# Kernel tuning notes

Measured on AMD Instinct MI355X. Metric: run time of the kernel, lower is better.

Reference implementation:

```python
import jax, jax.numpy as jnp
import numpy as np

SR = 44100
SEQ_DUR = 6.0
FBINS = 113
FMIN = 91.6
NSGT_SCALE = 100.0
MIN_WIN = 4


def _mel_frequencies(fmin, fmax, bnds):
    # MelScale from the nsgt package
    hz2mel = lambda f: 1127.01048 * np.log(f / 700.0 + 1.0)
    mel2hz = lambda m: (np.exp(m / 1127.01048) - 1.0) * 700.0
    mmin, mmax = hz2mel(fmin), hz2mel(fmax)
    mbnd = (mmax - mmin) / (bnds - 1)
    return mel2hz(np.arange(bnds) * mbnd + mmin)


def _hannwin(l):
    # fft-centered hann window (peak at index 0), as in nsgt.util.hannwin
    r = np.arange(l, dtype=np.float64) * (2.0 * np.pi / l)
    return 0.5 * (np.cos(r) + 1.0)


def _build_nsgt_params(Ls):
    """Replicates nsgfwin(sliced=False) + calcwinrange + matrixform nsgtf layout.
    Returns G[n_bins, maxLg] (window values, zero where padded) and
    idx[n_bins, maxLg] (gather indices into the length-Ls spectrum)."""
    f = _mel_frequencies(FMIN, SR / 2.0, FBINS)
    nf = SR / 2.0
    lim = int(np.argmax(f > 0))
    if lim != 0:
        f = f[lim:]
    lim = int(np.argmax(f >= nf))
    if lim != 0:
        f = f[:lim]
    lbas = len(f)
    frqs = np.concatenate(((0.0,), f, (nf,)))
    fbas = np.concatenate((frqs, SR - frqs[-2:0:-1]))
    fbas *= float(Ls) / SR
    # bandwidths M[k] (samples)
    M = np.zeros(fbas.shape, dtype=np.int64)
    M[0] = np.round(2 * fbas[1])
    for k in range(1, 2 * lbas + 1):
        M[k] = np.round(fbas[k + 1] - fbas[k - 1])
    M[-1] = np.round(Ls - fbas[-2])
    M = np.clip(M, MIN_WIN, None)
    g = [_hannwin(m) for m in M]
    fbas[lbas] = (fbas[lbas - 1] + fbas[lbas + 1]) / 2
    fbas[lbas + 2] = Ls - fbas[lbas]
    rfbas = np.round(fbas).astype(np.int64)  # window center positions (= timepos)
    # real=True, reducedform=0 -> keep bins 0 .. len(g)//2 (DC..Nyquist)
    n_bins = len(g) // 2 + 1
    maxLg = int(M.max())  # matrixform: every bin padded (in the middle) to max bandwidth
    idx = np.zeros((n_bins, maxLg), dtype=np.int32)
    G = np.zeros((n_bins, maxLg), dtype=np.float32)
    for j in range(n_bins):
        gj = g[j]
        Lg = len(gj)
        tp = int(rfbas[j])
        h = (Lg + 1) // 2  # positive-frequency half
        nh = Lg // 2       # negative-frequency half
        idx[j, :h] = (tp + np.arange(h)) % Ls
        G[j, :h] = gj[:h]
        if nh > 0:
            idx[j, maxLg - nh:] = (tp - nh + np.arange(nh)) % Ls
            G[j, maxLg - nh:] = gj[h:]
    return G, idx


def setup_inputs() -> dict:
    key = jax.random.key(0)
    S, C = 16, 2
    Ls = int(SEQ_DUR * SR)
    x = jax.random.normal(key, (S, C, Ls), dtype=jnp.float32)
    G, idx = _build_nsgt_params(Ls)
    return {"x": x, "G": jnp.asarray(G), "idx": jnp.asarray(idx)}


def reference(x, G, idx):
    # x: (S, C, Ls); G, idx: (n_bins, maxLg)
    S, C, T = x.shape
    ft = jnp.fft.fft(x.reshape(S * C, T))      # (N, Ls) complex64
    c = ft[:, idx] * G                         # (N, n_bins, maxLg): windowed spectrum slices
    coefs = jnp.fft.ifft(c, axis=-1)           # per-bin time frames (matrixform NSGT coeffs)
    coefs = coefs.reshape(S, C, c.shape[1], c.shape[2])
    # torch.view_as_real + * NSGT_SCALE
    return jnp.stack([coefs.real, coefs.imag], axis=-1) * NSGT_SCALE
```

## Files before the change

### kernel.cpp

```cpp
#include <hip/hip_runtime.h>

#define TPB 256
#define TPF 1024
constexpr int LS = 264600;
constexpr int N1 = 525;
constexpr int N2 = 504;
constexpr int ROWS = 32;
constexpr int M_FFT = 16384;
constexpr float TWO_PI_F = 6.28318530717958647692f;
constexpr float PI_F     = 3.14159265358979323846f;

__device__ __forceinline__ int rev7(int x) { return (int)(__brev((unsigned)x) >> 25); }
__device__ __forceinline__ float2 cmul(float2 a, float2 b) {
    return make_float2(a.x * b.x - a.y * b.y, a.x * b.y + a.y * b.x);
}
__device__ __forceinline__ int sidx(int hi, int lo) {
    return (hi << 7) + (lo ^ (hi & 15));
}

__global__ void k0_scan(const float* __restrict__ G, int NL, int* __restrict__ hnh) {
    const int j = blockIdx.x;
    __shared__ int s_first, s_last;
    if (threadIdx.x == 0) { s_first = NL; s_last = -1; }
    __syncthreads();
    const float* Gj = G + (size_t)j * NL;
    for (int m = threadIdx.x; m < NL; m += blockDim.x) {
        if (Gj[m] == 0.0f) {
            atomicMin(&s_first, m);
            atomicMax(&s_last, m);
        }
    }
    __syncthreads();
    if (threadIdx.x == 0) {
        int h  = s_first;
        int nh = (s_last >= 0) ? (NL - 1 - s_last) : 0;
        hnh[2 * j]     = h;
        hnh[2 * j + 1] = nh;
    }
}

__global__ __launch_bounds__(TPB) void k1_dft525(const float* __restrict__ x,
                                                 float2* __restrict__ A) {
    const int n2 = blockIdx.x;
    const int r  = blockIdx.y;
    __shared__ float  xs[N1];
    __shared__ float2 ys[N1];
    __shared__ float2 w25[25];
    __shared__ float2 w21[21];
    const float* xr = x + (size_t)r * LS + n2;
    for (int t = threadIdx.x; t < N1; t += TPB) {
        xs[t] = xr[(size_t)t * N2];
    }
    if (threadIdx.x < 25) {
        float a = -TWO_PI_F * (float)threadIdx.x / 25.0f;
        float s, c; sincosf(a, &s, &c);
        w25[threadIdx.x] = make_float2(c, s);
    } else if (threadIdx.x >= 32 && threadIdx.x < 53) {
        int k = threadIdx.x - 32;
        float a = -TWO_PI_F * (float)k / 21.0f;
        float s, c; sincosf(a, &s, &c);
        w21[k] = make_float2(c, s);
    }
    __syncthreads();
    for (int i = threadIdx.x; i < N1; i += TPB) {
        int alpha = i % 25, b = i / 25;
        float re = 0.f, im = 0.f;
        int iw = 0, it = b;
        #pragma unroll
        for (int a = 0; a < 25; ++a) {
            float  v = xs[it];
            float2 w = w25[iw];
            re = fmaf(v, w.x, re);
            im = fmaf(v, w.y, im);
            it += 21;
            iw += alpha; if (iw >= 25) iw -= 25;
        }
        float ang = -TWO_PI_F * (float)(b * alpha) / (float)N1;
        float s, c; sincosf(ang, &s, &c);
        ys[i] = make_float2(re * c - im * s, re * s + im * c);
    }
    __syncthreads();
    for (int k = threadIdx.x; k < N1; k += TPB) {
        int alpha = k % 25, beta = k / 25;
        float re = 0.f, im = 0.f;
        int iw = 0, iy = alpha;
        #pragma unroll
        for (int b = 0; b < 21; ++b) {
            float2 v = ys[iy];
            float2 w = w21[iw];
            re = fmaf(v.x, w.x, re); re = fmaf(-v.y, w.y, re);
            im = fmaf(v.x, w.y, im); im = fmaf( v.y, w.x, im);
            iy += 25;
            iw += beta; if (iw >= 21) iw -= 21;
        }
        float ang = -TWO_PI_F * (float)(k * n2) / (float)LS;
        float s, c; sincosf(ang, &s, &c);
        A[((size_t)r * N1 + k) * N2 + n2] = make_float2(re * c - im * s, re * s + im * c);
    }
}

__global__ __launch_bounds__(TPB) void k2_dft504(float2* __restrict__ A) {
    const int k1 = blockIdx.x;
    const int r  = blockIdx.y;
    __shared__ float2 as[N2];
    __shared__ float2 ys[N2];
    __shared__ float2 w21[21];
    __shared__ float2 w24[24];
    float2* row = A + ((size_t)r * N1 + k1) * N2;
    for (int t = threadIdx.x; t < N2; t += TPB) as[t] = row[t];
    if (threadIdx.x < 21) {
        float a = -TWO_PI_F * (float)threadIdx.x / 21.0f;
        float s, c; sincosf(a, &s, &c);
        w21[threadIdx.x] = make_float2(c, s);
    } else if (threadIdx.x >= 32 && threadIdx.x < 56) {
        int k = threadIdx.x - 32;
        float a = -TWO_PI_F * (float)k / 24.0f;
        float s, c; sincosf(a, &s, &c);
        w24[k] = make_float2(c, s);
    }
    __syncthreads();
    for (int i = threadIdx.x; i < N2; i += TPB) {
        int alpha = i % 21, b = i / 21;
        float re = 0.f, im = 0.f;
        int iw = 0, it = b;
        #pragma unroll
        for (int a = 0; a < 21; ++a) {
            float2 v = as[it];
            float2 w = w21[iw];
            re = fmaf(v.x, w.x, re); re = fmaf(-v.y, w.y, re);
            im = fmaf(v.x, w.y, im); im = fmaf( v.y, w.x, im);
            it += 24;
            iw += alpha; if (iw >= 21) iw -= 21;
        }
        float ang = -TWO_PI_F * (float)(b * alpha) / (float)N2;
        float s, c; sincosf(ang, &s, &c);
        ys[i] = make_float2(re * c - im * s, re * s + im * c);
    }
    __syncthreads();
    for (int k = threadIdx.x; k < N2; k += TPB) {
        int alpha = k % 21, beta = k / 21;
        float re = 0.f, im = 0.f;
        int iw = 0, iy = alpha;
        #pragma unroll
        for (int b = 0; b < 24; ++b) {
            float2 v = ys[iy];
            float2 w = w24[iw];
            re = fmaf(v.x, w.x, re); re = fmaf(-v.y, w.y, re);
            im = fmaf(v.x, w.y, im); im = fmaf( v.y, w.x, im);
            iy += 21;
            iw += beta; if (iw >= 24) iw -= 24;
        }
        row[k] = make_float2(re, im);
    }
}

__global__ void k_setup(float2* __restrict__ kc, float2* __restrict__ bchirp,
                        float2* __restrict__ twg, int NL) {
    int t = blockIdx.x * blockDim.x + threadIdx.x;
    long long twoNL = 2LL * NL;
    if (t < M_FFT) {
        long long d = 0; bool act = false;
        if (t < NL)              { d = t;        act = true; }
        else if (t > M_FFT - NL) { d = t - M_FFT; act = true; }
        float2 v = make_float2(0.f, 0.f);
        if (act) {
            long long ph = (d * d) % twoNL;
            float th = -PI_F * (float)ph / (float)NL;
            float s, c; sincosf(th, &s, &c);
            v = make_float2(c, s);
        }
        kc[t] = v;
    } else {
        int n = t - M_FFT;
        if (n < NL) {
            long long ph = ((long long)n * n) % twoNL;
            float th = PI_F * (float)ph / (float)NL;
            float s, c; sincosf(th, &s, &c);
            bchirp[n] = make_float2(c, s);
        } else if (n < NL + 64) {
            int q = n - NL;
            float th = -TWO_PI_F * (float)q / 128.0f;
            float s, c; sincosf(th, &s, &c);
            twg[q] = make_float2(c, s);
        }
    }
}

__device__ void fft128_dif(float2 (*ld)[129], const float2* tw, int f, int q) {
    for (int ls = 6; ls >= 0; --ls) {
        int span = 1 << ls;
        for (int b = q; b < 64; b += 16) {
            int j = b & (span - 1);
            int g = b >> ls;
            int u = (g << (ls + 1)) + j;
            int v = u + span;
            float2 A = ld[f][u], B = ld[f][v];
            float2 s = make_float2(A.x + B.x, A.y + B.y);
            float2 d = make_float2(A.x - B.x, A.y - B.y);
            ld[f][u] = s;
            ld[f][v] = cmul(d, tw[j << (6 - ls)]);
        }
        __syncthreads();
    }
}

#define FFT_PROLOG                                                        \
    __shared__ float2 ld[16][129];                                        \
    __shared__ float2 tw[64];                                             \
    if (threadIdx.x < 64) {                                               \
        float th = -TWO_PI_F * (float)threadIdx.x / 128.0f;               \
        float s, c; sincosf(th, &s, &c);                                  \
        tw[threadIdx.x] = make_float2(c, s);                              \
    }

__global__ __launch_bounds__(TPB) void kfft_cols_fwd(float2* __restrict__ P) {
    const int cg = blockIdx.x;
    const size_t vb = (size_t)blockIdx.y * M_FFT;
    FFT_PROLOG
    const int c0 = cg * 16;
    for (int i = threadIdx.x; i < 2048; i += TPB) {
        int cl = i & 15, r = i >> 4;
        ld[cl][r] = P[vb + (c0 + cl) + 128 * r];
    }
    __syncthreads();
    fft128_dif(ld, tw, threadIdx.x >> 4, threadIdx.x & 15);
    for (int i = threadIdx.x; i < 2048; i += TPB) {
        int cl = i & 15, pos = i >> 4;
        int c = c0 + cl;
        int k1 = rev7(pos);
        float th = -TWO_PI_F * (float)(c * k1) / (float)M_FFT;
        float s, co; sincosf(th, &s, &co);
        P[vb + c + 128 * pos] = cmul(ld[cl][pos], make_float2(co, s));
    }
}

__global__ __launch_bounds__(TPB) void kfft_rows_fwd(float2* __restrict__ P) {
    const int rg = blockIdx.x;
    const size_t vb = (size_t)blockIdx.y * M_FFT;
    FFT_PROLOG
    const int R0 = rg * 16;
    for (int i = threadIdx.x; i < 2048; i += TPB) {
        int fl = i >> 7, c = i & 127;
        ld[fl][c] = P[vb + (size_t)(R0 + fl) * 128 + c];
    }
    __syncthreads();
    fft128_dif(ld, tw, threadIdx.x >> 4, threadIdx.x & 15);
    for (int i = threadIdx.x; i < 2048; i += TPB) {
        int fl = i >> 7, pos = i & 127;
        P[vb + (size_t)(R0 + fl) * 128 + pos] = ld[fl][pos];
    }
}

__global__ __launch_bounds__(TPF) void k_fused(const float* __restrict__ Gm,
        const int* __restrict__ idxp, const float2* __restrict__ A,
        const int* __restrict__ hnh, const float2* __restrict__ bchirp,
        const float2* __restrict__ KF, const float2* __restrict__ twg,
        float2* __restrict__ out, int NB, int NL) {
    extern __shared__ float2 mp[];
    const int tid = threadIdx.x;
    const int vg = blockIdx.x;
    const int r = vg / NB, j = vg % NB;
    const int h = hnh[2 * j], nh = hnh[2 * j + 1];
    const int tail0 = NL - nh;
    const float* Gj = Gm + (size_t)j * NL;
    const int*   ij = idxp + (size_t)j * NL;
    const float2* Ar = A + (size_t)r * LS;

    for (int i = tid; i < M_FFT; i += TPF) {
        float2 val = make_float2(0.f, 0.f);
        if (i < h || (i >= tail0 && i < NL)) {
            int k = ij[i];
            float2 f = Ar[(size_t)(k % N1) * N2 + (k / N1)];
            float  g = Gj[i];
            val = cmul(make_float2(f.x * g, f.y * g), bchirp[i]);
        }
        mp[sidx(i >> 7, i & 127)] = val;
    }
    __syncthreads();

    for (int ls = 6; ls >= 0; --ls) {
        const int span = 1 << ls;
        for (int w = tid; w < 8192; w += TPF) {
            const int lo = w & 127, b = w >> 7;
            const int jj = b & (span - 1), g = b >> ls;
            const int u = (g << (ls + 1)) + jj, v = u + span;
            float2 Aa = mp[sidx(u, lo)], Bb = mp[sidx(v, lo)];
            float2 s = make_float2(Aa.x + Bb.x, Aa.y + Bb.y);
            float2 d = make_float2(Aa.x - Bb.x, Aa.y - Bb.y);
            mp[sidx(u, lo)] = s;
            mp[sidx(v, lo)] = cmul(d, twg[jj << (6 - ls)]);
        }
        __syncthreads();
    }
    for (int i = tid; i < M_FFT; i += TPF) {
        const int c = i & 127, pos = i >> 7;
        const int k1 = rev7(pos);
        float th = -TWO_PI_F * (float)(c * k1) / (float)M_FFT;
        float s, co; sincosf(th, &s, &co);
        const int p = sidx(pos, c);
        mp[p] = cmul(mp[p], make_float2(co, s));
    }
    __syncthreads();
    for (int ls = 6; ls >= 0; --ls) {
        const int span = 1 << ls;
        for (int w = tid; w < 8192; w += TPF) {
            const int hi = w & 127, b = w >> 7;
            const int jj = b & (span - 1), g = b >> ls;
            const int u = (g << (ls + 1)) + jj, v = u + span;
            float2 Aa = mp[sidx(hi, u)], Bb = mp[sidx(hi, v)];
            float2 s = make_float2(Aa.x + Bb.x, Aa.y + Bb.y);
            float2 d = make_float2(Aa.x - Bb.x, Aa.y - Bb.y);
            mp[sidx(hi, u)] = s;
            mp[sidx(hi, v)] = cmul(d, twg[jj << (6 - ls)]);
        }
        __syncthreads();
    }
    for (int i = tid; i < M_FFT; i += TPF) {
        const int p = sidx(i >> 7, i & 127);
        mp[p] = cmul(mp[p], KF[i]);
    }
    __syncthreads();
    for (int ls = 0; ls <= 6; ++ls) {
        const int span = 1 << ls;
        for (int w = tid; w < 8192; w += TPF) {
            const int hi = w & 127, b = w >> 7;
            const int jj = b & (span - 1), g = b >> ls;
            const int u = (g << (ls + 1)) + jj, v = u + span;
            float2 wv = twg[jj << (6 - ls)]; wv.y = -wv.y;
            float2 Aa = mp[sidx(hi, u)];
            float2 t  = cmul(mp[sidx(hi, v)], wv);
            mp[sidx(hi, u)] = make_float2(Aa.x + t.x, Aa.y + t.y);
            mp[sidx(hi, v)] = make_float2(Aa.x - t.x, Aa.y - t.y);
        }
        __syncthreads();
    }
    for (int i = tid; i < M_FFT; i += TPF) {
        const int pos = i & 127, R = i >> 7;
        const int k1 = rev7(R);
        float th = TWO_PI_F * (float)(k1 * pos) / (float)M_FFT;
        float s, co; sincosf(th, &s, &co);
        const int p = sidx(R, pos);
        mp[p] = cmul(mp[p], make_float2(co, s));
    }
    __syncthreads();
    for (int ls = 0; ls <= 6; ++ls) {
        const int span = 1 << ls;
        for (int w = tid; w < 8192; w += TPF) {
            const int lo = w & 127, b = w >> 7;
            const int jj = b & (span - 1), g = b >> ls;
            const int u = (g << (ls + 1)) + jj, v = u + span;
            float2 wv = twg[jj << (6 - ls)]; wv.y = -wv.y;
            float2 Aa = mp[sidx(u, lo)];
            float2 t  = cmul(mp[sidx(v, lo)], wv);
            mp[sidx(u, lo)] = make_float2(Aa.x + t.x, Aa.y + t.y);
            mp[sidx(v, lo)] = make_float2(Aa.x - t.x, Aa.y - t.y);
        }
        __syncthreads();
    }
    const float sc = 100.0f / ((float)NL * (float)M_FFT);
    float2* outv = out + (size_t)vg * NL;
    for (int n = tid; n < NL; n += TPF) {
        float2 y = cmul(mp[sidx(n >> 7, n & 127)], bchirp[n]);
        outv[n] = make_float2(y.x * sc, y.y * sc);
    }
}

__global__ __launch_bounds__(TPB) void k3_idft(const float* __restrict__ G,
                                               const int*  __restrict__ idxp,
                                               const float2* __restrict__ FT,
                                               const int*  __restrict__ hnh,
                                               float2* __restrict__ out,
                                               int NB, int NL) {
    extern __shared__ float2 cls[];
    const int j = blockIdx.x;
    const int r = blockIdx.y;
    const int h  = hnh[2 * j];
    const int nh = hnh[2 * j + 1];
    const int Lg = h + nh;
    const float* Gj = G    + (size_t)j * NL;
    const int*   ij = idxp + (size_t)j * NL;

    for (int t = threadIdx.x; t < Lg; t += TPB) {
        int m = (t < h) ? t : (NL - nh + (t - h));
        int k = ij[m];
        float2 f = FT[((size_t)r * N1 + (k % N1)) * N2 + (k / N1)];
        float  g = Gj[m];
        cls[t] = make_float2(f.x * g, f.y * g);
    }
    __syncthreads();

    const float scale = 100.0f / (float)NL;
    const float w0 = TWO_PI_F / (float)NL;
    float2* outr = out + ((size_t)r * NB + j) * NL;

    for (int n_base = 0; n_base < NL; n_base += 4 * TPB) {
        int   n[4];
        float are[4], aim[4], twr[4], twi[4], str[4], sti[4];
        #pragma unroll
        for (int u = 0; u < 4; ++u) {
            n[u] = n_base + u * TPB + (int)threadIdx.x;
            are[u] = 0.f; aim[u] = 0.f;
            float s, c; sincosf(w0 * (float)(n[u] % NL), &s, &c);
            str[u] = c; sti[u] = s;
            twr[u] = 1.f; twi[u] = 0.f;
        }
        for (int t = 0; t < h; ++t) {
            if ((t & 255) == 0) {
                #pragma unroll
                for (int u = 0; u < 4; ++u) {
                    int mm = (int)(((long long)t * (long long)n[u]) % NL);
                    float s, c; sincosf(w0 * (float)mm, &s, &c);
                    twr[u] = c; twi[u] = s;
                }
            }
            float2 cv = cls[t];
            #pragma unroll
            for (int u = 0; u < 4; ++u) {
                are[u] = fmaf(cv.x, twr[u], are[u]);
                are[u] = fmaf(-cv.y, twi[u], are[u]);
                aim[u] = fmaf(cv.x, twi[u], aim[u]);
                aim[u] = fmaf(cv.y, twr[u], aim[u]);
                float nr = twr[u] * str[u] - twi[u] * sti[u];
                float ni = twr[u] * sti[u] + twi[u] * str[u];
                twr[u] = nr; twi[u] = ni;
            }
        }
        const int m0 = NL - nh;
        for (int t = 0; t < nh; ++t) {
            if ((t & 255) == 0) {
                #pragma unroll
                for (int u = 0; u < 4; ++u) {
                    int mm = (int)(((long long)(m0 + t) * (long long)n[u]) % NL);
                    float s, c; sincosf(w0 * (float)mm, &s, &c);
                    twr[u] = c; twi[u] = s;
                }
            }
            float2 cv = cls[h + t];
            #pragma unroll
            for (int u = 0; u < 4; ++u) {
                are[u] = fmaf(cv.x, twr[u], are[u]);
                are[u] = fmaf(-cv.y, twi[u], are[u]);
                aim[u] = fmaf(cv.x, twi[u], aim[u]);
                aim[u] = fmaf(cv.y, twr[u], aim[u]);
                float nr = twr[u] * str[u] - twi[u] * sti[u];
                float ni = twr[u] * sti[u] + twi[u] * str[u];
                twr[u] = nr; twi[u] = ni;
            }
        }
        #pragma unroll
        for (int u = 0; u < 4; ++u) {
            if (n[u] < NL) outr[n[u]] = make_float2(are[u] * scale, aim[u] * scale);
        }
    }
}

static inline size_t align256(size_t x) { return (x + 255) & ~(size_t)255; }

extern "C" void kernel_launch(void* const* d_in, const int* in_sizes, int n_in,
                              void* d_out, int out_size, void* d_ws, size_t ws_size,
                              hipStream_t stream) {
    const float* x   = (const float*)d_in[0];
    const float* Gm  = (const float*)d_in[1];
    const int*   idx = (const int*)d_in[2];
    float2*      out = (float2*)d_out;

    const int p  = in_sizes[1];
    const int NB = (p % 114 == 0) ? 114 : 115;
    const int NL = p / NB;
    const int B  = NB * ROWS;

    size_t hnh_off    = 0;
    size_t bchirp_off = align256(hnh_off + 2048);
    size_t twg_off    = align256(bchirp_off + (size_t)NL * 8);
    size_t kc_off     = align256(twg_off + 64 * 8);
    size_t A_off      = align256(kc_off + (size_t)M_FFT * 8);
    size_t need       = A_off + (size_t)ROWS * LS * 8;

    int*    hnh    = (int*)((char*)d_ws + hnh_off);
    float2* bchirp = (float2*)((char*)d_ws + bchirp_off);
    float2* twg    = (float2*)((char*)d_ws + twg_off);
    float2* kc     = (float2*)((char*)d_ws + kc_off);
    float2* A      = (float2*)((char*)d_ws + A_off);

    k0_scan<<<dim3(NB), TPB, 0, stream>>>(Gm, NL, hnh);
    k1_dft525<<<dim3(N2, ROWS), TPB, 0, stream>>>(x, A);
    k2_dft504<<<dim3(N1, ROWS), TPB, 0, stream>>>(A);

    const bool fused_ok = (2 * NL - 1 <= M_FFT) && (need <= ws_size);
    if (fused_ok) {
        (void)hipFuncSetAttribute((const void*)k_fused,
                                  hipFuncAttributeMaxDynamicSharedMemorySize,
                                  M_FFT * (int)sizeof(float2));
        int setup_blocks = (M_FFT + NL + 64 + TPB - 1) / TPB;
        k_setup<<<dim3(setup_blocks), TPB, 0, stream>>>(kc, bchirp, twg, NL);
        kfft_cols_fwd<<<dim3(8, 1), TPB, 0, stream>>>(kc);
        kfft_rows_fwd<<<dim3(8, 1), TPB, 0, stream>>>(kc);
        k_fused<<<dim3(B), TPF, (size_t)M_FFT * sizeof(float2), stream>>>(
            Gm, idx, A, hnh, bchirp, kc, twg, out, NB, NL);
    } else {
        k3_idft<<<dim3(NB, ROWS), TPB, (size_t)NL * sizeof(float2), stream>>>(
            Gm, idx, A, hnh, out, NB, NL);
    }
}
```

Baseline: 1.504 ms.

## Replace radix-2 shared-memory FFT stages with register radix-16/8 passes in Bluestein kernel

The fused Bluestein kernel previously ran 16384-point FFTs as 4x7 radix-2 stages, each doing a shared-memory round trip and a barrier. It now keeps 16 values per thread in registers and uses radix-16 then radix-8 butterflies per 128-point dimension, so there are far fewer LDS passes and syncs. The chirp-filter FFT is also computed by one new register-based kernel that stores a transposed KF, replacing two small kernels. The cost is much higher register pressure at 1024 threads per block, plus more complex index bookkeeping.

```diff
diff --git a/kernel.cpp b/kernel.cpp
--- a/kernel.cpp
+++ b/kernel.cpp
@@ -10,12 +10,223 @@
 constexpr float TWO_PI_F = 6.28318530717958647692f;
 constexpr float PI_F     = 3.14159265358979323846f;
 
-__device__ __forceinline__ int rev7(int x) { return (int)(__brev((unsigned)x) >> 25); }
 __device__ __forceinline__ float2 cmul(float2 a, float2 b) {
     return make_float2(a.x * b.x - a.y * b.y, a.x * b.y + a.y * b.x);
 }
 __device__ __forceinline__ int sidx(int hi, int lo) {
     return (hi << 7) + (lo ^ (hi & 15));
+}
+
+#define BFLY(u, w, C, S) do {                       \
+    float dx_ = (u).x - (w).x, dy_ = (u).y - (w).y; \
+    (u).x += (w).x; (u).y += (w).y;                 \
+    (w).x = dx_ * (C) - dy_ * (S);                  \
+    (w).y = dx_ * (S) + dy_ * (C);                  \
+} while (0)
+
+template<bool INV>
+__device__ __forceinline__ void fft16s(float2 &a0, float2 &a1, float2 &a2, float2 &a3,
+                                       float2 &a4, float2 &a5, float2 &a6, float2 &a7,
+                                       float2 &a8, float2 &a9, float2 &a10, float2 &a11,
+                                       float2 &a12, float2 &a13, float2 &a14, float2 &a15) {
+    constexpr float c1 = 0.92387953251128674f;
+    constexpr float s1 = 0.38268343236508977f;
+    constexpr float r2 = 0.70710678118654752f;
+    const float sg = INV ? 1.f : -1.f;
+    BFLY(a0, a8,  1.f, 0.f);
+    BFLY(a1, a9,  c1,  sg * s1);
+    BFLY(a2, a10, r2,  sg * r2);
+    BFLY(a3, a11, s1,  sg * c1);
+    BFLY(a4, a12, 0.f, sg * 1.f);
+    BFLY(a5, a13, -s1, sg * c1);
+    BFLY(a6, a14, -r2, sg * r2);
+    BFLY(a7, a15, -c1, sg * s1);
+    BFLY(a0, a4,  1.f, 0.f);
+    BFLY(a1, a5,  r2,  sg * r2);
+    BFLY(a2, a6,  0.f, sg * 1.f);
+    BFLY(a3, a7,  -r2, sg * r2);
+    BFLY(a8, a12, 1.f, 0.f);
+    BFLY(a9, a13, r2,  sg * r2);
+    BFLY(a10, a14, 0.f, sg * 1.f);
+    BFLY(a11, a15, -r2, sg * r2);
+    BFLY(a0, a2,  1.f, 0.f);
+    BFLY(a1, a3,  0.f, sg * 1.f);
+    BFLY(a4, a6,  1.f, 0.f);
+    BFLY(a5, a7,  0.f, sg * 1.f);
+    BFLY(a8, a10, 1.f, 0.f);
+    BFLY(a9, a11, 0.f, sg * 1.f);
+    BFLY(a12, a14, 1.f, 0.f);
+    BFLY(a13, a15, 0.f, sg * 1.f);
+    BFLY(a0, a1,  1.f, 0.f);
+    BFLY(a2, a3,  1.f, 0.f);
+    BFLY(a4, a5,  1.f, 0.f);
+    BFLY(a6, a7,  1.f, 0.f);
+    BFLY(a8, a9,  1.f, 0.f);
+    BFLY(a10, a11, 1.f, 0.f);
+    BFLY(a12, a13, 1.f, 0.f);
+    BFLY(a14, a15, 1.f, 0.f);
+}
+
+template<bool INV>
+__device__ __forceinline__ void fft8s(float2 &b0, float2 &b1, float2 &b2, float2 &b3,
+                                      float2 &b4, float2 &b5, float2 &b6, float2 &b7) {
+    constexpr float r2 = 0.70710678118654752f;
+    const float sg = INV ? 1.f : -1.f;
+    BFLY(b0, b4, 1.f, 0.f);
+    BFLY(b1, b5, r2,  sg * r2);
+    BFLY(b2, b6, 0.f, sg * 1.f);
+    BFLY(b3, b7, -r2, sg * r2);
+    BFLY(b0, b2, 1.f, 0.f);
+    BFLY(b1, b3, 0.f, sg * 1.f);
+    BFLY(b4, b6, 1.f, 0.f);
+    BFLY(b5, b7, 0.f, sg * 1.f);
+    BFLY(b0, b1, 1.f, 0.f);
+    BFLY(b2, b3, 1.f, 0.f);
+    BFLY(b4, b5, 1.f, 0.f);
+    BFLY(b6, b7, 1.f, 0.f);
+}
+
+#define CTW(w) make_float2((w).x, -(w).y)
+
+#define STW_FWD(var, rr) do {                                              \
+    float th_ = -TWO_PI_F * (float)((rr) * lo) / (float)M_FFT;             \
+    float s_, c_; sincosf(th_, &s_, &c_);                                  \
+    mp[sidx((rr), lo)] = cmul((var), make_float2(c_, s_));                 \
+} while (0)
+
+#define STW_INV(var, bc) do {                                              \
+    float th_ = TWO_PI_F * (float)((bc) * hi) / (float)M_FFT;              \
+    float s_, c_; sincosf(th_, &s_, &c_);                                  \
+    mp[sidx(hi, (bc))] = cmul((var), make_float2(c_, s_));                 \
+} while (0)
+
+__device__ __forceinline__ void fwd_core(float2* __restrict__ mp,
+        const float2* __restrict__ twg, const int lo, const int n2,
+        float2 &a0, float2 &a1, float2 &a2, float2 &a3,
+        float2 &a4, float2 &a5, float2 &a6, float2 &a7,
+        float2 &a8, float2 &a9, float2 &a10, float2 &a11,
+        float2 &a12, float2 &a13, float2 &a14, float2 &a15) {
+    fft16s<false>(a0, a1, a2, a3, a4, a5, a6, a7, a8, a9, a10, a11, a12, a13, a14, a15);
+    mp[sidx(n2,       lo)] = a0;
+    mp[sidx(64 + n2,  lo)] = cmul(a1,  twg[n2 * 8]);
+    mp[sidx(32 + n2,  lo)] = cmul(a2,  twg[n2 * 4]);
+    mp[sidx(96 + n2,  lo)] = cmul(a3,  twg[n2 * 12]);
+    mp[sidx(16 + n2,  lo)] = cmul(a4,  twg[n2 * 2]);
+    mp[sidx(80 + n2,  lo)] = cmul(a5,  twg[n2 * 10]);
+    mp[sidx(48 + n2,  lo)] = cmul(a6,  twg[n2 * 6]);
+    mp[sidx(112 + n2, lo)] = cmul(a7,  twg[n2 * 14]);
+    mp[sidx(8 + n2,   lo)] = cmul(a8,  twg[n2 * 1]);
+    mp[sidx(72 + n2,  lo)] = cmul(a9,  twg[n2 * 9]);
+    mp[sidx(40 + n2,  lo)] = cmul(a10, twg[n2 * 5]);
+    mp[sidx(104 + n2, lo)] = cmul(a11, twg[n2 * 13]);
+    mp[sidx(24 + n2,  lo)] = cmul(a12, twg[n2 * 3]);
+    mp[sidx(88 + n2,  lo)] = cmul(a13, twg[n2 * 11]);
+    mp[sidx(56 + n2,  lo)] = cmul(a14, twg[n2 * 7]);
+    mp[sidx(120 + n2, lo)] = cmul(a15, twg[n2 * 15]);
+    __syncthreads();
+    {
+        float2 b0 = mp[sidx(8 * n2 + 0, lo)];
+        float2 b1 = mp[sidx(8 * n2 + 1, lo)];
+        float2 b2 = mp[sidx(8 * n2 + 2, lo)];
+        float2 b3 = mp[sidx(8 * n2 + 3, lo)];
+        float2 b4 = mp[sidx(8 * n2 + 4, lo)];
+        float2 b5 = mp[sidx(8 * n2 + 5, lo)];
+        float2 b6 = mp[sidx(8 * n2 + 6, lo)];
+        float2 b7 = mp[sidx(8 * n2 + 7, lo)];
+        float2 c0 = mp[sidx(8 * n2 + 64, lo)];
+        float2 c1 = mp[sidx(8 * n2 + 65, lo)];
+        float2 c2 = mp[sidx(8 * n2 + 66, lo)];
+        float2 c3 = mp[sidx(8 * n2 + 67, lo)];
+        float2 c4 = mp[sidx(8 * n2 + 68, lo)];
+        float2 c5 = mp[sidx(8 * n2 + 69, lo)];
+        float2 c6 = mp[sidx(8 * n2 + 70, lo)];
+        float2 c7 = mp[sidx(8 * n2 + 71, lo)];
+        __syncthreads();
+        fft8s<false>(b0, b1, b2, b3, b4, b5, b6, b7);
+        fft8s<false>(c0, c1, c2, c3, c4, c5, c6, c7);
+        STW_FWD(b0, n2 + 0);  STW_FWD(b1, n2 + 64);
+        STW_FWD(b2, n2 + 32); STW_FWD(b3, n2 + 96);
+        STW_FWD(b4, n2 + 16); STW_FWD(b5, n2 + 80);
+        STW_FWD(b6, n2 + 48); STW_FWD(b7, n2 + 112);
+        STW_FWD(c0, n2 + 8);  STW_FWD(c1, n2 + 72);
+        STW_FWD(c2, n2 + 40); STW_FWD(c3, n2 + 104);
+        STW_FWD(c4, n2 + 24); STW_FWD(c5, n2 + 88);
+        STW_FWD(c6, n2 + 56); STW_FWD(c7, n2 + 120);
+    }
+    __syncthreads();
+    const int hi = lo;
+    a0  = mp[sidx(hi, n2)];
+    a1  = mp[sidx(hi, 8 + n2)];
+    a2  = mp[sidx(hi, 16 + n2)];
+    a3  = mp[sidx(hi, 24 + n2)];
+    a4  = mp[sidx(hi, 32 + n2)];
+    a5  = mp[sidx(hi, 40 + n2)];
+    a6  = mp[sidx(hi, 48 + n2)];
+    a7  = mp[sidx(hi, 56 + n2)];
+    a8  = mp[sidx(hi, 64 + n2)];
+    a9  = mp[sidx(hi, 72 + n2)];
+    a10 = mp[sidx(hi, 80 + n2)];
+    a11 = mp[sidx(hi, 88 + n2)];
+    a12 = mp[sidx(hi, 96 + n2)];
+    a13 = mp[sidx(hi, 104 + n2)];
+    a14 = mp[sidx(hi, 112 + n2)];
+    a15 = mp[sidx(hi, 120 + n2)];
+    fft16s<false>(a0, a1, a2, a3, a4, a5, a6, a7, a8, a9, a10, a11, a12, a13, a14, a15);
+    mp[sidx(hi, n2)]       = a0;
+    mp[sidx(hi, 64 + n2)]  = cmul(a1,  twg[n2 * 8]);
+    mp[sidx(hi, 32 + n2)]  = cmul(a2,  twg[n2 * 4]);
+    mp[sidx(hi, 96 + n2)]  = cmul(a3,  twg[n2 * 12]);
+    mp[sidx(hi, 16 + n2)]  = cmul(a4,  twg[n2 * 2]);
+    mp[sidx(hi, 80 + n2)]  = cmul(a5,  twg[n2 * 10]);
+    mp[sidx(hi, 48 + n2)]  = cmul(a6,  twg[n2 * 6]);
+    mp[sidx(hi, 112 + n2)] = cmul(a7,  twg[n2 * 14]);
+    mp[sidx(hi, 8 + n2)]   = cmul(a8,  twg[n2 * 1]);
+    mp[sidx(hi, 72 + n2)]  = cmul(a9,  twg[n2 * 9]);
+    mp[sidx(hi, 40 + n2)]  = cmul(a10, twg[n2 * 5]);
+    mp[sidx(hi, 104 + n2)] = cmul(a11, twg[n2 * 13]);
+    mp[sidx(hi, 24 + n2)]  = cmul(a12, twg[n2 * 3]);
+    mp[sidx(hi, 88 + n2)]  = cmul(a13, twg[n2 * 11]);
+    mp[sidx(hi, 56 + n2)]  = cmul(a14, twg[n2 * 7]);
+    mp[sidx(hi, 120 + n2)] = cmul(a15, twg[n2 * 15]);
+    __syncthreads();
+    {
+        float2 b0 = mp[sidx(hi, 8 * n2 + 0)];
+        float2 b1 = mp[sidx(hi, 8 * n2 + 1)];
+        float2 b2 = mp[sidx(hi, 8 * n2 + 2)];
+        float2 b3 = mp[sidx(hi, 8 * n2 + 3)];
+        float2 b4 = mp[sidx(hi, 8 * n2 + 4)];
+        float2 b5 = mp[sidx(hi, 8 * n2 + 5)];
+        float2 b6 = mp[sidx(hi, 8 * n2 + 6)];
+        float2 b7 = mp[sidx(hi, 8 * n2 + 7)];
+        float2 c0 = mp[sidx(hi, 8 * n2 + 64)];
+        float2 c1 = mp[sidx(hi, 8 * n2 + 65)];
+        float2 c2 = mp[sidx(hi, 8 * n2 + 66)];
+        float2 c3 = mp[sidx(hi, 8 * n2 + 67)];
+        float2 c4 = mp[sidx(hi, 8 * n2 + 68)];
+        float2 c5 = mp[sidx(hi, 8 * n2 + 69)];
+        float2 c6 = mp[sidx(hi, 8 * n2 + 70)];
+        float2 c7 = mp[sidx(hi, 8 * n2 + 71)];
+        __syncthreads();
+        fft8s<false>(b0, b1, b2, b3, b4, b5, b6, b7);
+        fft8s<false>(c0, c1, c2, c3, c4, c5, c6, c7);
+        mp[sidx(hi, n2 + 0)]   = b0;
+        mp[sidx(hi, n2 + 64)]  = b1;
+        mp[sidx(hi, n2 + 32)]  = b2;
+        mp[sidx(hi, n2 + 96)]  = b3;
+        mp[sidx(hi, n2 + 16)]  = b4;
+        mp[sidx(hi, n2 + 80)]  = b5;
+        mp[sidx(hi, n2 + 48)]  = b6;
+        mp[sidx(hi, n2 + 112)] = b7;
+        mp[sidx(hi, n2 + 8)]   = c0;
+        mp[sidx(hi, n2 + 72)]  = c1;
+        mp[sidx(hi, n2 + 40)]  = c2;
+        mp[sidx(hi, n2 + 104)] = c3;
+        mp[sidx(hi, n2 + 24)]  = c4;
+        mp[sidx(hi, n2 + 88)]  = c5;
+        mp[sidx(hi, n2 + 56)]  = c6;
+        mp[sidx(hi, n2 + 120)] = c7;
+    }
+    __syncthreads();
 }
 
 __global__ void k0_scan(const float* __restrict__ G, int NL, int* __restrict__ hnh) {
@@ -177,7 +388,7 @@
             float th = PI_F * (float)ph / (float)NL;
             float s, c; sincosf(th, &s, &c);
             bchirp[n] = make_float2(c, s);
-        } else if (n < NL + 64) {
+        } else if (n < NL + 128) {
             int q = n - NL;
             float th = -TWO_PI_F * (float)q / 128.0f;
             float s, c; sincosf(th, &s, &c);
@@ -186,182 +397,218 @@
     }
 }
 
-__device__ void fft128_dif(float2 (*ld)[129], const float2* tw, int f, int q) {
-    for (int ls = 6; ls >= 0; --ls) {
-        int span = 1 << ls;
-        for (int b = q; b < 64; b += 16) {
-            int j = b & (span - 1);
-            int g = b >> ls;
-            int u = (g << (ls + 1)) + j;
-            int v = u + span;
-            float2 A = ld[f][u], B = ld[f][v];
-            float2 s = make_float2(A.x + B.x, A.y + B.y);
-            float2 d = make_float2(A.x - B.x, A.y - B.y);
-            ld[f][u] = s;
-            ld[f][v] = cmul(d, tw[j << (6 - ls)]);
-        }
-        __syncthreads();
-    }
-}
-
-#define FFT_PROLOG                                                        \
-    __shared__ float2 ld[16][129];                                        \
-    __shared__ float2 tw[64];                                             \
-    if (threadIdx.x < 64) {                                               \
-        float th = -TWO_PI_F * (float)threadIdx.x / 128.0f;               \
-        float s, c; sincosf(th, &s, &c);                                  \
-        tw[threadIdx.x] = make_float2(c, s);                              \
-    }
-
-__global__ __launch_bounds__(TPB) void kfft_cols_fwd(float2* __restrict__ P) {
-    const int cg = blockIdx.x;
-    const size_t vb = (size_t)blockIdx.y * M_FFT;
-    FFT_PROLOG
-    const int c0 = cg * 16;
-    for (int i = threadIdx.x; i < 2048; i += TPB) {
-        int cl = i & 15, r = i >> 4;
-        ld[cl][r] = P[vb + (c0 + cl) + 128 * r];
-    }
-    __syncthreads();
-    fft128_dif(ld, tw, threadIdx.x >> 4, threadIdx.x & 15);
-    for (int i = threadIdx.x; i < 2048; i += TPB) {
-        int cl = i & 15, pos = i >> 4;
-        int c = c0 + cl;
-        int k1 = rev7(pos);
-        float th = -TWO_PI_F * (float)(c * k1) / (float)M_FFT;
-        float s, co; sincosf(th, &s, &co);
-        P[vb + c + 128 * pos] = cmul(ld[cl][pos], make_float2(co, s));
-    }
-}
-
-__global__ __launch_bounds__(TPB) void kfft_rows_fwd(float2* __restrict__ P) {
-    const int rg = blockIdx.x;
-    const size_t vb = (size_t)blockIdx.y * M_FFT;
-    FFT_PROLOG
-    const int R0 = rg * 16;
-    for (int i = threadIdx.x; i < 2048; i += TPB) {
-        int fl = i >> 7, c = i & 127;
-        ld[fl][c] = P[vb + (size_t)(R0 + fl) * 128 + c];
-    }
-    __syncthreads();
-    fft128_dif(ld, tw, threadIdx.x >> 4, threadIdx.x & 15);
-    for (int i = threadIdx.x; i < 2048; i += TPB) {
-        int fl = i >> 7, pos = i & 127;
-        P[vb + (size_t)(R0 + fl) * 128 + pos] = ld[fl][pos];
-    }
-}
+__global__ __launch_bounds__(TPF) void k_kf(const float2* __restrict__ kc,
+        const float2* __restrict__ twg, float2* __restrict__ KFt) {
+    extern __shared__ float2 mp[];
+    const int tid = threadIdx.x;
+    const int lo = tid & 127, n2 = tid >> 7;
+    float2 a0  = kc[tid];
+    float2 a1  = kc[1024 + tid];
+    float2 a2  = kc[2048 + tid];
+    float2 a3  = kc[3072 + tid];
+    float2 a4  = kc[4096 + tid];
+    float2 a5  = kc[5120 + tid];
+    float2 a6  = kc[6144 + tid];
+    float2 a7  = kc[7168 + tid];
+    float2 a8  = kc[8192 + tid];
+    float2 a9  = kc[9216 + tid];
+    float2 a10 = kc[10240 + tid];
+    float2 a11 = kc[11264 + tid];
+    float2 a12 = kc[12288 + tid];
+    float2 a13 = kc[13312 + tid];
+    float2 a14 = kc[14336 + tid];
+    float2 a15 = kc[15360 + tid];
+    fwd_core(mp, twg, lo, n2, a0, a1, a2, a3, a4, a5, a6, a7,
+             a8, a9, a10, a11, a12, a13, a14, a15);
+    for (int i = tid; i < M_FFT; i += TPF) {
+        int hh = i >> 7, ll = i & 127;
+        KFt[(size_t)ll * 128 + hh] = mp[sidx(hh, ll)];
+    }
+}
+
+#define GATH(var, I) do {                                                     \
+    (var) = make_float2(0.f, 0.f);                                            \
+    const int i_ = (I);                                                       \
+    if (i_ < h || (i_ >= tail0 && i_ < NL)) {                                 \
+        int k_ = ij[i_];                                                      \
+        float2 f_ = Ar[(size_t)(k_ % N1) * N2 + (k_ / N1)];                   \
+        float  g_ = Gj[i_];                                                   \
+        (var) = cmul(make_float2(f_.x * g_, f_.y * g_), bchirp[i_]);          \
+    }                                                                         \
+} while (0)
+
+#define FINST(var, acol) do {                                                 \
+    const int n_ = 128 * (acol) + lo;                                         \
+    if (n_ < NL) {                                                            \
+        float2 y_ = cmul((var), bchirp[n_]);                                  \
+        outv[n_] = make_float2(y_.x * sc, y_.y * sc);                         \
+    }                                                                         \
+} while (0)
 
 __global__ __launch_bounds__(TPF) void k_fused(const float* __restrict__ Gm,
         const int* __restrict__ idxp, const float2* __restrict__ A,
         const int* __restrict__ hnh, const float2* __restrict__ bchirp,
-        const float2* __restrict__ KF, const float2* __restrict__ twg,
+        const float2* __restrict__ KFt, const float2* __restrict__ twg,
         float2* __restrict__ out, int NB, int NL) {
     extern __shared__ float2 mp[];
     const int tid = threadIdx.x;
+    const int lo = tid & 127, n2 = tid >> 7;
     const int vg = blockIdx.x;
-    const int r = vg / NB, j = vg % NB;
-    const int h = hnh[2 * j], nh = hnh[2 * j + 1];
+    const int rr_ = vg / NB, jb = vg % NB;
+    const int h = hnh[2 * jb], nh = hnh[2 * jb + 1];
     const int tail0 = NL - nh;
-    const float* Gj = Gm + (size_t)j * NL;
-    const int*   ij = idxp + (size_t)j * NL;
-    const float2* Ar = A + (size_t)r * LS;
-
-    for (int i = tid; i < M_FFT; i += TPF) {
-        float2 val = make_float2(0.f, 0.f);
-        if (i < h || (i >= tail0 && i < NL)) {
-            int k = ij[i];
-            float2 f = Ar[(size_t)(k % N1) * N2 + (k / N1)];
-            float  g = Gj[i];
-            val = cmul(make_float2(f.x * g, f.y * g), bchirp[i]);
-        }
-        mp[sidx(i >> 7, i & 127)] = val;
-    }
-    __syncthreads();
-
-    for (int ls = 6; ls >= 0; --ls) {
-        const int span = 1 << ls;
-        for (int w = tid; w < 8192; w += TPF) {
-            const int lo = w & 127, b = w >> 7;
-            const int jj = b & (span - 1), g = b >> ls;
-            const int u = (g << (ls + 1)) + jj, v = u + span;
-            float2 Aa = mp[sidx(u, lo)], Bb = mp[sidx(v, lo)];
-            float2 s = make_float2(Aa.x + Bb.x, Aa.y + Bb.y);
-            float2 d = make_float2(Aa.x - Bb.x, Aa.y - Bb.y);
-            mp[sidx(u, lo)] = s;
-            mp[sidx(v, lo)] = cmul(d, twg[jj << (6 - ls)]);
-        }
+    const float* Gj = Gm + (size_t)jb * NL;
+    const int*   ij = idxp + (size_t)jb * NL;
+    const float2* Ar = A + (size_t)rr_ * LS;
+
+    float2 a0, a1, a2, a3, a4, a5, a6, a7, a8, a9, a10, a11, a12, a13, a14, a15;
+    GATH(a0, tid);
+    GATH(a1, 1024 + tid);
+    GATH(a2, 2048 + tid);
+    GATH(a3, 3072 + tid);
+    GATH(a4, 4096 + tid);
+    GATH(a5, 5120 + tid);
+    GATH(a6, 6144 + tid);
+    GATH(a7, 7168 + tid);
+    GATH(a8, 8192 + tid);
+    GATH(a9, 9216 + tid);
+    GATH(a10, 10240 + tid);
+    GATH(a11, 11264 + tid);
+    GATH(a12, 12288 + tid);
+    GATH(a13, 13312 + tid);
+    GATH(a14, 14336 + tid);
+    GATH(a15, 15360 + tid);
+    fwd_core(mp, twg, lo, n2, a0, a1, a2, a3, a4, a5, a6, a7,
+             a8, a9, a10, a11, a12, a13, a14, a15);
+
+    const int hi = lo;
+    a0  = cmul(mp[sidx(hi, n2)],       KFt[(size_t)(n2) * 128 + hi]);
+    a1  = cmul(mp[sidx(hi, 8 + n2)],   KFt[(size_t)(8 + n2) * 128 + hi]);
+    a2  = cmul(mp[sidx(hi, 16 + n2)],  KFt[(size_t)(16 + n2) * 128 + hi]);
+    a3  = cmul(mp[sidx(hi, 24 + n2)],  KFt[(size_t)(24 + n2) * 128 + hi]);
+    a4  = cmul(mp[sidx(hi, 32 + n2)],  KFt[(size_t)(32 + n2) * 128 + hi]);
+    a5  = cmul(mp[sidx(hi, 40 + n2)],  KFt[(size_t)(40 + n2) * 128 + hi]);
+    a6  = cmul(mp[sidx(hi, 48 + n2)],  KFt[(size_t)(48 + n2) * 128 + hi]);
+    a7  = cmul(mp[sidx(hi, 56 + n2)],  KFt[(size_t)(56 + n2) * 128 + hi]);
+    a8  = cmul(mp[sidx(hi, 64 + n2)],  KFt[(size_t)(64 + n2) * 128 + hi]);
+    a9  = cmul(mp[sidx(hi, 72 + n2)],  KFt[(size_t)(72 + n2) * 128 + hi]);
+    a10 = cmul(mp[sidx(hi, 80 + n2)],  KFt[(size_t)(80 + n2) * 128 + hi]);
+    a11 = cmul(mp[sidx(hi, 88 + n2)],  KFt[(size_t)(88 + n2) * 128 + hi]);
+    a12 = cmul(mp[sidx(hi, 96 + n2)],  KFt[(size_t)(96 + n2) * 128 + hi]);
+    a13 = cmul(mp[sidx(hi, 104 + n2)], KFt[(size_t)(104 + n2) * 128 + hi]);
+    a14 = cmul(mp[sidx(hi, 112 + n2)], KFt[(size_t)(112 + n2) * 128 + hi]);
+    a15 = cmul(mp[sidx(hi, 120 + n2)], KFt[(size_t)(120 + n2) * 128 + hi]);
+    fft16s<true>(a0, a1, a2, a3, a4, a5, a6, a7, a8, a9, a10, a11, a12, a13, a14, a15);
+    mp[sidx(hi, n2)]       = a0;
+    mp[sidx(hi, 64 + n2)]  = cmul(a1,  CTW(twg[n2 * 8]));
+    mp[sidx(hi, 32 + n2)]  = cmul(a2,  CTW(twg[n2 * 4]));
+    mp[sidx(hi, 96 + n2)]  = cmul(a3,  CTW(twg[n2 * 12]));
+    mp[sidx(hi, 16 + n2)]  = cmul(a4,  CTW(twg[n2 * 2]));
+    mp[sidx(hi, 80 + n2)]  = cmul(a5,  CTW(twg[n2 * 10]));
+    mp[sidx(hi, 48 + n2)]  = cmul(a6,  CTW(twg[n2 * 6]));
+    mp[sidx(hi, 112 + n2)] = cmul(a7,  CTW(twg[n2 * 14]));
+    mp[sidx(hi, 8 + n2)]   = cmul(a8,  CTW(twg[n2 * 1]));
+    mp[sidx(hi, 72 + n2)]  = cmul(a9,  CTW(twg[n2 * 9]));
+    mp[sidx(hi, 40 + n2)]  = cmul(a10, CTW(twg[n2 * 5]));
+    mp[sidx(hi, 104 + n2)] = cmul(a11, CTW(twg[n2 * 13]));
+    mp[sidx(hi, 24 + n2)]  = cmul(a12, CTW(twg[n2 * 3]));
+    mp[sidx(hi, 88 + n2)]  = cmul(a13, CTW(twg[n2 * 11]));
+    mp[sidx(hi, 56 + n2)]  = cmul(a14, CTW(twg[n2 * 7]));
+    mp[sidx(hi, 120 + n2)] = cmul(a15, CTW(twg[n2 * 15]));
+    __syncthreads();
+    {
+        float2 b0 = mp[sidx(hi, 8 * n2 + 0)];
+        float2 b1 = mp[sidx(hi, 8 * n2 + 1)];
+        float2 b2 = mp[sidx(hi, 8 * n2 + 2)];
+        float2 b3 = mp[sidx(hi, 8 * n2 + 3)];
+        float2 b4 = mp[sidx(hi, 8 * n2 + 4)];
+        float2 b5 = mp[sidx(hi, 8 * n2 + 5)];
+        float2 b6 = mp[sidx(hi, 8 * n2 + 6)];
+        float2 b7 = mp[sidx(hi, 8 * n2 + 7)];
+        float2 c0 = mp[sidx(hi, 8 * n2 + 64)];
+        float2 c1 = mp[sidx(hi, 8 * n2 + 65)];
+        float2 c2 = mp[sidx(hi, 8 * n2 + 66)];
+        float2 c3 = mp[sidx(hi, 8 * n2 + 67)];
+        float2 c4 = mp[sidx(hi, 8 * n2 + 68)];
+        float2 c5 = mp[sidx(hi, 8 * n2 + 69)];
+        float2 c6 = mp[sidx(hi, 8 * n2 + 70)];
+        float2 c7 = mp[sidx(hi, 8 * n2 + 71)];
         __syncthreads();
-    }
-    for (int i = tid; i < M_FFT; i += TPF) {
-        const int c = i & 127, pos = i >> 7;
-        const int k1 = rev7(pos);
-        float th = -TWO_PI_F * (float)(c * k1) / (float)M_FFT;
-        float s, co; sincosf(th, &s, &co);
-        const int p = sidx(pos, c);
-        mp[p] = cmul(mp[p], make_float2(co, s));
-    }
-    __syncthreads();
-    for (int ls = 6; ls >= 0; --ls) {
-        const int span = 1 << ls;
-        for (int w = tid; w < 8192; w += TPF) {
-            const int hi = w & 127, b = w >> 7;
-            const int jj = b & (span - 1), g = b >> ls;
-            const int u = (g << (ls + 1)) + jj, v = u + span;
-            float2 Aa = mp[sidx(hi, u)], Bb = mp[sidx(hi, v)];
-            float2 s = make_float2(Aa.x + Bb.x, Aa.y + Bb.y);
-            float2 d = make_float2(Aa.x - Bb.x, Aa.y - Bb.y);
-            mp[sidx(hi, u)] = s;
-            mp[sidx(hi, v)] = cmul(d, twg[jj << (6 - ls)]);
-        }
-        __syncthreads();
-    }
-    for (int i = tid; i < M_FFT; i += TPF) {
-        const int p = sidx(i >> 7, i & 127);
-        mp[p] = cmul(mp[p], KF[i]);
-    }
-    __syncthreads();
-    for (int ls = 0; ls <= 6; ++ls) {
-        const int span = 1 << ls;
-        for (int w = tid; w < 8192; w += TPF) {
-            const int hi = w & 127, b = w >> 7;
-            const int jj = b & (span - 1), g = b >> ls;
-            const int u = (g << (ls + 1)) + jj, v = u + span;
-            float2 wv = twg[jj << (6 - ls)]; wv.y = -wv.y;
-            float2 Aa = mp[sidx(hi, u)];
-            float2 t  = cmul(mp[sidx(hi, v)], wv);
-            mp[sidx(hi, u)] = make_float2(Aa.x + t.x, Aa.y + t.y);
-            mp[sidx(hi, v)] = make_float2(Aa.x - t.x, Aa.y - t.y);
-        }
-        __syncthreads();
-    }
-    for (int i = tid; i < M_FFT; i += TPF) {
-        const int pos = i & 127, R = i >> 7;
-        const int k1 = rev7(R);
-        float th = TWO_PI_F * (float)(k1 * pos) / (float)M_FFT;
-        float s, co; sincosf(th, &s, &co);
-        const int p = sidx(R, pos);
-        mp[p] = cmul(mp[p], make_float2(co, s));
-    }
-    __syncthreads();
-    for (int ls = 0; ls <= 6; ++ls) {
-        const int span = 1 << ls;
-        for (int w = tid; w < 8192; w += TPF) {
-            const int lo = w & 127, b = w >> 7;
-            const int jj = b & (span - 1), g = b >> ls;
-            const int u = (g << (ls + 1)) + jj, v = u + span;
-            float2 wv = twg[jj << (6 - ls)]; wv.y = -wv.y;
-            float2 Aa = mp[sidx(u, lo)];
-            float2 t  = cmul(mp[sidx(v, lo)], wv);
-            mp[sidx(u, lo)] = make_float2(Aa.x + t.x, Aa.y + t.y);
-            mp[sidx(v, lo)] = make_float2(Aa.x - t.x, Aa.y - t.y);
-        }
-        __syncthreads();
-    }
-    const float sc = 100.0f / ((float)NL * (float)M_FFT);
-    float2* outv = out + (size_t)vg * NL;
-    for (int n = tid; n < NL; n += TPF) {
-        float2 y = cmul(mp[sidx(n >> 7, n & 127)], bchirp[n]);
-        outv[n] = make_float2(y.x * sc, y.y * sc);
+        fft8s<true>(b0, b1, b2, b3, b4, b5, b6, b7);
+        fft8s<true>(c0, c1, c2, c3, c4, c5, c6, c7);
+        STW_INV(b0, n2 + 0);  STW_INV(b1, n2 + 64);
+        STW_INV(b2, n2 + 32); STW_INV(b3, n2 + 96);
+        STW_INV(b4, n2 + 16); STW_INV(b5, n2 + 80);
+        STW_INV(b6, n2 + 48); STW_INV(b7, n2 + 112);
+        STW_INV(c0, n2 + 8);  STW_INV(c1, n2 + 72);
+        STW_INV(c2, n2 + 40); STW_INV(c3, n2 + 104);
+        STW_INV(c4, n2 + 24); STW_INV(c5, n2 + 88);
+        STW_INV(c6, n2 + 56); STW_INV(c7, n2 + 120);
+    }
+    __syncthreads();
+    a0  = mp[sidx(n2, lo)];
+    a1  = mp[sidx(8 + n2, lo)];
+    a2  = mp[sidx(16 + n2, lo)];
+    a3  = mp[sidx(24 + n2, lo)];
+    a4  = mp[sidx(32 + n2, lo)];
+    a5  = mp[sidx(40 + n2, lo)];
+    a6  = mp[sidx(48 + n2, lo)];
+    a7  = mp[sidx(56 + n2, lo)];
+    a8  = mp[sidx(64 + n2, lo)];
+    a9  = mp[sidx(72 + n2, lo)];
+    a10 = mp[sidx(80 + n2, lo)];
+    a11 = mp[sidx(88 + n2, lo)];
+    a12 = mp[sidx(96 + n2, lo)];
+    a13 = mp[sidx(104 + n2, lo)];
+    a14 = mp[sidx(112 + n2, lo)];
+    a15 = mp[sidx(120 + n2, lo)];
+    fft16s<true>(a0, a1, a2, a3, a4, a5, a6, a7, a8, a9, a10, a11, a12, a13, a14, a15);
+    mp[sidx(n2, lo)]       = a0;
+    mp[sidx(64 + n2, lo)]  = cmul(a1,  CTW(twg[n2 * 8]));
+    mp[sidx(32 + n2, lo)]  = cmul(a2,  CTW(twg[n2 * 4]));
+    mp[sidx(96 + n2, lo)]  = cmul(a3,  CTW(twg[n2 * 12]));
+    mp[sidx(16 + n2, lo)]  = cmul(a4,  CTW(twg[n2 * 2]));
+    mp[sidx(80 + n2, lo)]  = cmul(a5,  CTW(twg[n2 * 10]));
+    mp[sidx(48 + n2, lo)]  = cmul(a6,  CTW(twg[n2 * 6]));
+    mp[sidx(112 + n2, lo)] = cmul(a7,  CTW(twg[n2 * 14]));
+    mp[sidx(8 + n2, lo)]   = cmul(a8,  CTW(twg[n2 * 1]));
+    mp[sidx(72 + n2, lo)]  = cmul(a9,  CTW(twg[n2 * 9]));
+    mp[sidx(40 + n2, lo)]  = cmul(a10, CTW(twg[n2 * 5]));
+    mp[sidx(104 + n2, lo)] = cmul(a11, CTW(twg[n2 * 13]));
+    mp[sidx(24 + n2, lo)]  = cmul(a12, CTW(twg[n2 * 3]));
+    mp[sidx(88 + n2, lo)]  = cmul(a13, CTW(twg[n2 * 11]));
+    mp[sidx(56 + n2, lo)]  = cmul(a14, CTW(twg[n2 * 7]));
+    mp[sidx(120 + n2, lo)] = cmul(a15, CTW(twg[n2 * 15]));
+    __syncthreads();
+    {
+        float2 b0 = mp[sidx(8 * n2 + 0, lo)];
+        float2 b1 = mp[sidx(8 * n2 + 1, lo)];
+        float2 b2 = mp[sidx(8 * n2 + 2, lo)];
+        float2 b3 = mp[sidx(8 * n2 + 3, lo)];
+        float2 b4 = mp[sidx(8 * n2 + 4, lo)];
+        float2 b5 = mp[sidx(8 * n2 + 5, lo)];
+        float2 b6 = mp[sidx(8 * n2 + 6, lo)];
+        float2 b7 = mp[sidx(8 * n2 + 7, lo)];
+        float2 c0 = mp[sidx(8 * n2 + 64, lo)];
+        float2 c1 = mp[sidx(8 * n2 + 65, lo)];
+        float2 c2 = mp[sidx(8 * n2 + 66, lo)];
+        float2 c3 = mp[sidx(8 * n2 + 67, lo)];
+        float2 c4 = mp[sidx(8 * n2 + 68, lo)];
+        float2 c5 = mp[sidx(8 * n2 + 69, lo)];
+        float2 c6 = mp[sidx(8 * n2 + 70, lo)];
+        float2 c7 = mp[sidx(8 * n2 + 71, lo)];
+        fft8s<true>(b0, b1, b2, b3, b4, b5, b6, b7);
+        fft8s<true>(c0, c1, c2, c3, c4, c5, c6, c7);
+        const float sc = 100.0f / ((float)NL * (float)M_FFT);
+        float2* outv = out + (size_t)vg * NL;
+        FINST(b0, n2 + 0);  FINST(b1, n2 + 64);
+        FINST(b2, n2 + 32); FINST(b3, n2 + 96);
+        FINST(b4, n2 + 16); FINST(b5, n2 + 80);
+        FINST(b6, n2 + 48); FINST(b7, n2 + 112);
+        FINST(c0, n2 + 8);  FINST(c1, n2 + 72);
+        FINST(c2, n2 + 40); FINST(c3, n2 + 104);
+        FINST(c4, n2 + 24); FINST(c5, n2 + 88);
+        FINST(c6, n2 + 56); FINST(c7, n2 + 120);
     }
 }
 
@@ -472,14 +719,16 @@
     size_t hnh_off    = 0;
     size_t bchirp_off = align256(hnh_off + 2048);
     size_t twg_off    = align256(bchirp_off + (size_t)NL * 8);
-    size_t kc_off     = align256(twg_off + 64 * 8);
-    size_t A_off      = align256(kc_off + (size_t)M_FFT * 8);
+    size_t kc_off     = align256(twg_off + 128 * 8);
+    size_t kft_off    = align256(kc_off + (size_t)M_FFT * 8);
+    size_t A_off      = align256(kft_off + (size_t)M_FFT * 8);
     size_t need       = A_off + (size_t)ROWS * LS * 8;
 
     int*    hnh    = (int*)((char*)d_ws + hnh_off);
     float2* bchirp = (float2*)((char*)d_ws + bchirp_off);
     float2* twg    = (float2*)((char*)d_ws + twg_off);
     float2* kc     = (float2*)((char*)d_ws + kc_off);
+    float2* KFt    = (float2*)((char*)d_ws + kft_off);
     float2* A      = (float2*)((char*)d_ws + A_off);
 
     k0_scan<<<dim3(NB), TPB, 0, stream>>>(Gm, NL, hnh);
@@ -491,12 +740,14 @@
         (void)hipFuncSetAttribute((const void*)k_fused,
                                   hipFuncAttributeMaxDynamicSharedMemorySize,
                                   M_FFT * (int)sizeof(float2));
-        int setup_blocks = (M_FFT + NL + 64 + TPB - 1) / TPB;
+        (void)hipFuncSetAttribute((const void*)k_kf,
+                                  hipFuncAttributeMaxDynamicSharedMemorySize,
+                                  M_FFT * (int)sizeof(float2));
+        int setup_blocks = (M_FFT + NL + 128 + TPB - 1) / TPB;
         k_setup<<<dim3(setup_blocks), TPB, 0, stream>>>(kc, bchirp, twg, NL);
-        kfft_cols_fwd<<<dim3(8, 1), TPB, 0, stream>>>(kc);
-        kfft_rows_fwd<<<dim3(8, 1), TPB, 0, stream>>>(kc);
+        k_kf<<<dim3(1), TPF, (size_t)M_FFT * sizeof(float2), stream>>>(kc, twg, KFt);
         k_fused<<<dim3(B), TPF, (size_t)M_FFT * sizeof(float2), stream>>>(
-            Gm, idx, A, hnh, bchirp, kc, twg, out, NB, NL);
+            Gm, idx, A, hnh, bchirp, KFt, twg, out, NB, NL);
     } else {
         k3_idft<<<dim3(NB, ROWS), TPB, (size_t)NL * sizeof(float2), stream>>>(
             Gm, idx, A, hnh, out, NB, NL);
```

Measured after the change: 1.625 ms. 8.0% more time.
